# Kernel optimization log

Hardware: AMD Instinct MI355X
Metric: run time of the kernel (lower is better)

## Reference

```python
import jax, jax.numpy as jnp
import numpy as np

N, NFEAT, NHID, OUT, E, P = 50000, 256, 128, 64, 800000, 3
WALK_STEPS, LAMBDA_RW = 13, 0.2


def spmm(row, col, val, x):
    # sparse (N,N) @ dense (N,d) via gather + segment-sum over destination rows
    return jax.ops.segment_sum(val[:, None] * x[col], row, num_segments=N)


def telu(x):
    return x * jnp.tanh(jnp.exp(x))


def setup_inputs() -> dict:
    key = jax.random.key(0)
    ks = jax.random.split(key, 24)
    s = 0.05
    inp = {
        'feature': jax.random.normal(ks[0], (N, NFEAT), jnp.float32),
        'edge_index': jax.random.randint(ks[1], (P, 2, E), 0, N, jnp.int64),
        'edge_val': jax.random.uniform(ks[2], (P, E), jnp.float32) / 16.0,
        'spec_w1': jax.random.normal(ks[3], (P, NFEAT, NHID)) * s,
        'spec_b1': jax.random.normal(ks[4], (P, NHID)) * s,
        'spec_w2': jax.random.normal(ks[5], (P, NHID, OUT)) * s,
        'spec_b2': jax.random.normal(ks[6], (P, OUT)) * s,
        'shared_w1': jax.random.normal(ks[7], (NFEAT, NHID)) * s,
        'shared_b1': jax.random.normal(ks[8], (NHID,)) * s,
        'shared_w2': jax.random.normal(ks[9], (NHID, OUT)) * s,
        'shared_b2': jax.random.normal(ks[10], (OUT,)) * s,
        'weight_b': jax.random.normal(ks[11], (P, 1)) * s,
        'tau': jnp.float32(0.5),
        'mlp_w1': jax.random.normal(ks[12], (OUT * P, NHID)) * s,
        'mlp_b1': jax.random.normal(ks[13], (NHID,)) * s,
        'mlp_w2': jax.random.normal(ks[14], (NHID, OUT)) * s,
        'mlp_b2': jax.random.normal(ks[15], (OUT,)) * s,
        'raw_w1': jax.random.normal(ks[16], (NFEAT, OUT)) * s,
        'raw_b1': jax.random.normal(ks[17], (OUT,)) * s,
        'raw_w2': jax.random.normal(ks[18], (OUT, OUT)) * s,
        'raw_b2': jax.random.normal(ks[19], (OUT,)) * s,
        'proj_w': jax.random.normal(ks[20], (OUT * 4, OUT)) * s,
        'proj_b': jax.random.normal(ks[21], (OUT,)) * s,
    }
    return inp


def reference(feature, edge_index, edge_val, spec_w1, spec_b1, spec_w2, spec_b2,
              shared_w1, shared_b1, shared_w2, shared_b2, weight_b, tau,
              mlp_w1, mlp_b1, mlp_w2, mlp_b2, raw_w1, raw_b1, raw_w2, raw_b2,
              proj_w, proj_b):
    rows = [edge_index[i, 0] for i in range(P)]
    cols = [edge_index[i, 1] for i in range(P)]
    vals = [edge_val[i] for i in range(P)]

    def gc(x, w, b, i):
        return spmm(rows[i], cols[i], vals[i], x @ w) + b

    # path-specific two-layer GCNs (dropout in eval mode = identity)
    specific = []
    for i in range(P):
        h1 = telu(gc(feature, spec_w1[i], spec_b1[i], i))
        specific.append(gc(h1, spec_w2[i], spec_b2[i], i))
    spec_stack = jnp.stack(specific, axis=0)  # (P, N, OUT)

    # shared GCN applied per path
    shared = []
    for i in range(P):
        h1 = telu(gc(feature, shared_w1, shared_b1, i))
        shared.append(gc(h1, shared_w2, shared_b2, i))
    shared_stack = jnp.stack(shared, axis=0)
    H_sh = jnp.mean(shared_stack, axis=0)

    # markov-enhanced path attention
    summaries = []
    for s in specific:
        mean_pool = s.mean(axis=0)
        max_pool = s.max(axis=0)
        p = jax.nn.softmax(s, axis=0)
        entropy = -jnp.sum(p * jnp.log(p + 1e-6), axis=0)
        summaries.append(jnp.concatenate([mean_pool, max_pool, entropy], axis=-1))
    ps = jnp.stack(summaries, axis=0)  # (P, 3*OUT)
    sim = (ps @ ps.T) / (jnp.sqrt(jnp.float32(3 * OUT)) * tau)
    T = jax.nn.softmax(sim, axis=1)
    pi0 = jax.nn.softmax(weight_b.squeeze(-1), axis=0)
    pi = pi0
    for _ in range(WALK_STEPS):
        pi = LAMBDA_RW * pi0 + (1.0 - LAMBDA_RW) * (pi @ T)
    W_tilde = pi[:, None]  # beta dropout is identity in eval mode

    # collaborative MLP on concatenated specific features
    concat_sp = jnp.concatenate(specific, axis=1)  # (N, P*OUT)
    H_col = jax.nn.relu(concat_sp @ mlp_w1 + mlp_b1) @ mlp_w2 + mlp_b2

    # attention-fused specific features
    wprob = jax.nn.softmax(W_tilde, axis=0)[:, 0]  # (P,)
    H_sp_fused = jnp.einsum('pnd,p->nd', spec_stack, wprob)

    # raw path on merged adjacency: final_A = sum_i W_tilde[i] * A_i (applied lazily)
    w = W_tilde[:, 0]

    def merged_spmm(x):
        acc = jnp.zeros((N, x.shape[1]), x.dtype)
        for i in range(P):
            acc = acc + w[i] * spmm(rows[i], cols[i], vals[i], x)
        return acc

    U1 = merged_spmm(feature @ raw_w1) + raw_b1
    U2 = merged_spmm(U1 @ raw_w2) + raw_b2
    H_raw = (U1 + U2) / 2.0

    all_feat = jnp.concatenate([H_sp_fused, H_sh, H_col, H_raw], axis=1)
    out = all_feat @ proj_w + proj_b
    return (out, spec_stack, shared_stack, H_col, H_raw)
```

## Files before the change

### kernel.cpp

```cpp
#include <hip/hip_runtime.h>
#include <hip/hip_bf16.h>
#include <math.h>

#define NN 50000
#define NFEAT 256
#define NHID 128
#define OUTD 64
#define NE 800000
#define NP 3
#define NCH 64
#define RC 782
#define NSB 196
#define NNR (NN + 1)

typedef __hip_bfloat16 bf16;
typedef __attribute__((ext_vector_type(8))) short short8;
typedef __attribute__((ext_vector_type(4))) short short4v;
typedef __attribute__((ext_vector_type(4))) float f32x4;

static inline int cdiv(long a, long b) { return (int)((a + b - 1) / b); }

__device__ __forceinline__ short f2bf(float x) {
    unsigned u = __builtin_bit_cast(unsigned, x);
    unsigned r = (u + 0x7FFFu + ((u >> 16) & 1u)) >> 16;
    return (short)r;
}
__device__ __forceinline__ float bf2f(short b) {
    unsigned u = ((unsigned)(unsigned short)b) << 16;
    return __builtin_bit_cast(float, u);
}

__device__ __forceinline__ void ld8(const float* __restrict__ p, float v[8]) {
    float4 a = *reinterpret_cast<const float4*>(p);
    float4 b = *reinterpret_cast<const float4*>(p + 4);
    v[0] = a.x; v[1] = a.y; v[2] = a.z; v[3] = a.w;
    v[4] = b.x; v[5] = b.y; v[6] = b.z; v[7] = b.w;
}

__device__ __forceinline__ void store4(float* p, const float o[4]) {
    *reinterpret_cast<float4*>(p) = make_float4(o[0], o[1], o[2], o[3]);
}
__device__ __forceinline__ void store4(bf16* p, const float o[4]) {
    short4v u;
    u[0] = f2bf(o[0]); u[1] = f2bf(o[1]); u[2] = f2bf(o[2]); u[3] = f2bf(o[3]);
    *reinterpret_cast<short4v*>(p) = u;
}

__global__ void transpose_split(const float* __restrict__ src, bf16* __restrict__ dh,
                                bf16* __restrict__ dl, int K, int M, long total) {
    long idx = (long)blockIdx.x * blockDim.x + threadIdx.x;
    if (idx >= total) return;
    long pm = idx / K;
    int k = (int)(idx - pm * K);
    long p = pm / M;
    int m = (int)(pm - p * M);
    float v = src[(p * K + k) * M + m];
    short hb = f2bf(v);
    short lb = f2bf(v - bf2f(hb));
    reinterpret_cast<short*>(dh)[idx] = hb;
    reinterpret_cast<short*>(dl)[idx] = lb;
}

template <int K, int M, int MODE, int ACT, typename OT>
__global__ __launch_bounds__(256) void gemm_mfma(
    const float* __restrict__ A, const bf16* __restrict__ Bh, const bf16* __restrict__ Bl,
    const float* __restrict__ bias, OT* __restrict__ out, int nrows,
    const float* __restrict__ wvec, const float* __restrict__ s1,
    const float* __restrict__ s2, const float* __restrict__ s3) {
    constexpr int MC = M / 16;
    __shared__ short AsH[64 * 32];
    __shared__ short AsL[64 * 32];

    int t = threadIdx.x;
    int n0 = blockIdx.x * 64;
    int w = t >> 6;
    int l = t & 63;
    int lr = l & 15, lq = l >> 4;

    float w0 = 0.f, w1 = 0.f, w2 = 0.f;
    if (MODE == 2) { w0 = wvec[3]; w1 = wvec[4]; w2 = wvec[5]; }

    f32x4 acc[MC];
#pragma unroll
    for (int i = 0; i < MC; ++i) {
        f32x4 z = {0.f, 0.f, 0.f, 0.f};
        acc[i] = z;
    }

    int sr = t >> 2, sc = t & 3;
    int gn_s = n0 + sr;
    int wslot = (sc ^ ((sr >> 2) & 3)) << 3;
    short* wpH = &AsH[sr * 32 + wslot];
    short* wpL = &AsL[sr * 32 + wslot];

    int rrow = (w << 4) + lr;
    int roff = rrow * 32 + ((lq ^ ((rrow >> 2) & 3)) << 3);
    const short* rpH = &AsH[roff];
    const short* rpL = &AsL[roff];

    const short* Bhs = reinterpret_cast<const short*>(Bh);
    const short* Bls = reinterpret_cast<const short*>(Bl);

    auto loadA = [&](int k0, float v[8]) {
        if (gn_s >= nrows) {
#pragma unroll
            for (int j = 0; j < 8; ++j) v[j] = 0.f;
            return;
        }
        if (MODE == 0) {
            ld8(A + (long)gn_s * K + k0 + sc * 8, v);
        } else if (MODE == 1) {
            int plane = k0 >> 6;
            int d = (k0 & 63) + sc * 8;
            ld8(A + ((long)plane * NN + gn_s) * OUTD + d, v);
        } else {
            int seg = k0 >> 6;
            int d = (k0 & 63) + sc * 8;
            if (seg == 0) {
                float x0[8], x1[8], x2[8];
                ld8(A + ((long)0 * NN + gn_s) * OUTD + d, x0);
                ld8(A + ((long)1 * NN + gn_s) * OUTD + d, x1);
                ld8(A + ((long)2 * NN + gn_s) * OUTD + d, x2);
#pragma unroll
                for (int j = 0; j < 8; ++j) v[j] = w0 * x0[j] + w1 * x1[j] + w2 * x2[j];
            } else if (seg == 1) {
                float x0[8], x1[8], x2[8];
                ld8(s1 + ((long)0 * NN + gn_s) * OUTD + d, x0);
                ld8(s1 + ((long)1 * NN + gn_s) * OUTD + d, x1);
                ld8(s1 + ((long)2 * NN + gn_s) * OUTD + d, x2);
#pragma unroll
                for (int j = 0; j < 8; ++j) v[j] = (x0[j] + x1[j] + x2[j]) * (1.0f / 3.0f);
            } else if (seg == 2) {
                ld8(s2 + (long)gn_s * OUTD + d, v);
            } else {
                ld8(s3 + (long)gn_s * OUTD + d, v);
            }
        }
    };

    float v[8];
    loadA(0, v);
    for (int k0 = 0; k0 < K; k0 += 32) {
        short8 ah, al;
#pragma unroll
        for (int j = 0; j < 8; ++j) {
            short hb = f2bf(v[j]);
            ah[j] = hb;
            al[j] = f2bf(v[j] - bf2f(hb));
        }
        __syncthreads();
        *reinterpret_cast<short8*>(wpH) = ah;
        *reinterpret_cast<short8*>(wpL) = al;
        __syncthreads();
        if (k0 + 32 < K) loadA(k0 + 32, v);
        short8 fah = *reinterpret_cast<const short8*>(rpH);
        short8 fal = *reinterpret_cast<const short8*>(rpL);
#pragma unroll
        for (int m = 0; m < MC; ++m) {
            long wb = (long)(m * 16 + lr) * K + k0 + (lq << 3);
            short8 bh = *reinterpret_cast<const short8*>(Bhs + wb);
            short8 bl = *reinterpret_cast<const short8*>(Bls + wb);
            acc[m] = __builtin_amdgcn_mfma_f32_16x16x32_bf16(bh, fah, acc[m], 0, 0, 0);
            acc[m] = __builtin_amdgcn_mfma_f32_16x16x32_bf16(bl, fah, acc[m], 0, 0, 0);
            acc[m] = __builtin_amdgcn_mfma_f32_16x16x32_bf16(bh, fal, acc[m], 0, 0, 0);
        }
    }

    int gn = n0 + (w << 4) + lr;
    if (gn < nrows) {
#pragma unroll
        for (int m = 0; m < MC; ++m) {
            int mb = m * 16 + (lq << 2);
            float o[4];
#pragma unroll
            for (int r = 0; r < 4; ++r) {
                o[r] = acc[m][r] + (bias ? bias[mb + r] : 0.f);
                if (ACT == 2) o[r] = fmaxf(o[r], 0.f);
            }
            store4(&out[(long)gn * M + mb], o);
        }
    }
}

__global__ void hist_all(const int* __restrict__ ei, int* __restrict__ cnt) {
    int p = blockIdx.y;
    int e = blockIdx.x * blockDim.x + threadIdx.x;
    if (e >= NE) return;
    int r = ei[((long)p * 2) * NE + e];
    atomicAdd(&cnt[(long)p * NN + r], 1);
}

__global__ void scan_pass1(const int* __restrict__ cnt, int* __restrict__ bsum) {
    int p = blockIdx.y, b = blockIdx.x, t = threadIdx.x;
    int idx = b * 256 + t;
    int v = (idx < NN) ? cnt[(long)p * NN + idx] : 0;
    __shared__ int sh[256];
    sh[t] = v;
    __syncthreads();
    for (int off = 128; off > 0; off >>= 1) {
        if (t < off) sh[t] += sh[t + off];
        __syncthreads();
    }
    if (t == 0) bsum[p * NSB + b] = sh[0];
}

__global__ void scan_pass2(const int* __restrict__ bsum, int* __restrict__ boff) {
    int p = blockIdx.x, t = threadIdx.x;
    int v = (t < NSB) ? bsum[p * NSB + t] : 0;
    __shared__ int sh[256];
    sh[t] = v;
    __syncthreads();
    for (int off = 1; off < 256; off <<= 1) {
        int tmp = (t >= off) ? sh[t - off] : 0;
        __syncthreads();
        sh[t] += tmp;
        __syncthreads();
    }
    if (t < NSB) boff[p * NSB + t] = sh[t] - v;
}

__global__ void scan_pass3(const int* __restrict__ cnt, const int* __restrict__ boff,
                           int* __restrict__ rowptr, int* __restrict__ cursor) {
    int p = blockIdx.y, b = blockIdx.x, t = threadIdx.x;
    int idx = b * 256 + t;
    int v = (idx < NN) ? cnt[(long)p * NN + idx] : 0;
    __shared__ int sh[256];
    sh[t] = v;
    __syncthreads();
    for (int off = 1; off < 256; off <<= 1) {
        int tmp = (t >= off) ? sh[t - off] : 0;
        __syncthreads();
        sh[t] += tmp;
        __syncthreads();
    }
    int rp = boff[p * NSB + b] + sh[t] - v;
    if (idx < NN) {
        rowptr[(long)p * NNR + idx] = rp;
        cursor[(long)p * NN + idx] = rp;
    }
    if (idx == NN - 1) rowptr[(long)p * NNR + NN] = rp + v;
}

__global__ void scatter_all(const int* __restrict__ ei, const float* __restrict__ ev,
                            int* __restrict__ cursor, int* __restrict__ csr_col,
                            float* __restrict__ csr_val) {
    int p = blockIdx.y;
    int e = blockIdx.x * blockDim.x + threadIdx.x;
    if (e >= NE) return;
    int r = ei[((long)p * 2) * NE + e];
    int c = ei[((long)p * 2 + 1) * NE + e];
    float v = ev[(long)p * NE + e];
    int pos = atomicAdd(&cursor[(long)p * NN + r], 1);
    csr_col[(long)p * NE + pos] = c;
    csr_val[(long)p * NE + pos] = v;
}

template <int M, int ACT, int RPB>
__global__ void spmm_dual(const int* __restrict__ rowptr, const int* __restrict__ ccol,
                          const float* __restrict__ cval,
                          const bf16* __restrict__ Ya, const bf16* __restrict__ Yb,
                          const float* __restrict__ biasA, const float* __restrict__ biasB,
                          float* __restrict__ outA, float* __restrict__ outB) {
    constexpr int TPR = M / 2;
    int t = threadIdx.x;
    int n = blockIdx.x * RPB + t / TPR;
    int hs = t % TPR;
    int h = hs * 2;
    if (n >= NN) return;
    int e0 = rowptr[n], e1 = rowptr[n + 1];
    float aAl = biasA[h], aAh = biasA[h + 1];
    float aBl = biasB[h], aBh = biasB[h + 1];
    const unsigned* Ua = reinterpret_cast<const unsigned*>(Ya);
    const unsigned* Ub = reinterpret_cast<const unsigned*>(Yb);
    int e = e0;
    for (; e + 3 < e1; e += 4) {
        int c0 = ccol[e], c1 = ccol[e + 1], c2 = ccol[e + 2], c3 = ccol[e + 3];
        float v0 = cval[e], v1 = cval[e + 1], v2 = cval[e + 2], v3 = cval[e + 3];
        unsigned a0 = Ua[(long)c0 * TPR + hs], a1 = Ua[(long)c1 * TPR + hs];
        unsigned a2 = Ua[(long)c2 * TPR + hs], a3 = Ua[(long)c3 * TPR + hs];
        unsigned b0 = Ub[(long)c0 * TPR + hs], b1 = Ub[(long)c1 * TPR + hs];
        unsigned b2 = Ub[(long)c2 * TPR + hs], b3 = Ub[(long)c3 * TPR + hs];
        aAl += v0 * bf2f((short)a0) + v1 * bf2f((short)a1) + v2 * bf2f((short)a2) + v3 * bf2f((short)a3);
        aAh += v0 * bf2f((short)(a0 >> 16)) + v1 * bf2f((short)(a1 >> 16)) +
               v2 * bf2f((short)(a2 >> 16)) + v3 * bf2f((short)(a3 >> 16));
        aBl += v0 * bf2f((short)b0) + v1 * bf2f((short)b1) + v2 * bf2f((short)b2) + v3 * bf2f((short)b3);
        aBh += v0 * bf2f((short)(b0 >> 16)) + v1 * bf2f((short)(b1 >> 16)) +
               v2 * bf2f((short)(b2 >> 16)) + v3 * bf2f((short)(b3 >> 16));
    }
    for (; e < e1; ++e) {
        int c = ccol[e];
        float v = cval[e];
        unsigned a = Ua[(long)c * TPR + hs];
        unsigned b = Ub[(long)c * TPR + hs];
        aAl += v * bf2f((short)a);
        aAh += v * bf2f((short)(a >> 16));
        aBl += v * bf2f((short)b);
        aBh += v * bf2f((short)(b >> 16));
    }
    if (ACT == 1) {
        aAl = aAl * tanhf(expf(aAl)); aAh = aAh * tanhf(expf(aAh));
        aBl = aBl * tanhf(expf(aBl)); aBh = aBh * tanhf(expf(aBh));
    }
    *reinterpret_cast<float2*>(&outA[(long)n * M + h]) = make_float2(aAl, aAh);
    *reinterpret_cast<float2*>(&outB[(long)n * M + h]) = make_float2(aBl, aBh);
}

__global__ void spmm_merged(const int* __restrict__ rp0, const int* __restrict__ cc0, const float* __restrict__ cv0,
                            const int* __restrict__ rp1, const int* __restrict__ cc1, const float* __restrict__ cv1,
                            const int* __restrict__ rp2, const int* __restrict__ cc2, const float* __restrict__ cv2,
                            const bf16* __restrict__ Y, const float* __restrict__ wvec,
                            const float* __restrict__ bias, float* __restrict__ out) {
    constexpr int TPR = 32;
    int t = threadIdx.x;
    int n = blockIdx.x * 2 + t / TPR;
    int hs = t % TPR;
    int h = hs * 2;
    if (n >= NN) return;
    const int* rps[3] = {rp0, rp1, rp2};
    const int* ccs[3] = {cc0, cc1, cc2};
    const float* cvs[3] = {cv0, cv1, cv2};
    const unsigned* U = reinterpret_cast<const unsigned*>(Y);
    float al = 0.f, ah = 0.f;
#pragma unroll
    for (int p = 0; p < 3; ++p) {
        const int* cc = ccs[p];
        const float* cv = cvs[p];
        int e0 = rps[p][n], e1 = rps[p][n + 1];
        float sl = 0.f, sh = 0.f;
        int e = e0;
        for (; e + 3 < e1; e += 4) {
            int c0 = cc[e], c1 = cc[e + 1], c2 = cc[e + 2], c3 = cc[e + 3];
            float v0 = cv[e], v1 = cv[e + 1], v2 = cv[e + 2], v3 = cv[e + 3];
            unsigned y0 = U[(long)c0 * TPR + hs], y1 = U[(long)c1 * TPR + hs];
            unsigned y2 = U[(long)c2 * TPR + hs], y3 = U[(long)c3 * TPR + hs];
            sl += v0 * bf2f((short)y0) + v1 * bf2f((short)y1) + v2 * bf2f((short)y2) + v3 * bf2f((short)y3);
            sh += v0 * bf2f((short)(y0 >> 16)) + v1 * bf2f((short)(y1 >> 16)) +
                  v2 * bf2f((short)(y2 >> 16)) + v3 * bf2f((short)(y3 >> 16));
        }
        for (; e < e1; ++e) {
            unsigned y = U[(long)cc[e] * TPR + hs];
            float v = cv[e];
            sl += v * bf2f((short)y);
            sh += v * bf2f((short)(y >> 16));
        }
        float wv = wvec[p];
        al += wv * sl;
        ah += wv * sh;
    }
    *reinterpret_cast<float2*>(&out[(long)n * OUTD + h]) =
        make_float2(al + bias[h], ah + bias[h + 1]);
}

__global__ void colsum_passA(const float* __restrict__ spec, float* __restrict__ pmax,
                             float* __restrict__ psum, float* __restrict__ pexp) {
    int p = blockIdx.y, c = blockIdx.x;
    int t = threadIdx.x;
    int d = t & 63, rg = t >> 6;
    const float* base = spec + (long)p * NN * OUTD;
    int r0 = c * RC, r1 = min(r0 + RC, NN);
    float m = -INFINITY, s = 0.f, e = 0.f;
    for (int r = r0 + rg; r < r1; r += 4) {
        float v = base[(long)r * OUTD + d];
        s += v;
        if (v > m) { e = e * __expf(m - v) + 1.0f; m = v; }
        else e += __expf(v - m);
    }
    __shared__ float rm[256], rs[256], re[256];
    rm[t] = m; rs[t] = s; re[t] = e;
    __syncthreads();
    for (int off = 128; off >= 64; off >>= 1) {
        if (t < off) {
            float m2 = fmaxf(rm[t], rm[t + off]);
            re[t] = re[t] * __expf(rm[t] - m2) + re[t + off] * __expf(rm[t + off] - m2);
            rm[t] = m2;
            rs[t] = rs[t] + rs[t + off];
        }
        __syncthreads();
    }
    if (t < 64) {
        long idx = ((long)p * 64 + t) * NCH + c;
        pmax[idx] = rm[t]; psum[idx] = rs[t]; pexp[idx] = re[t];
    }
}

__global__ void colsum_reduceB(const float* __restrict__ pmax, const float* __restrict__ psum,
                               const float* __restrict__ pexp, float* __restrict__ ps,
                               float* __restrict__ zbuf) {
    int b = blockIdx.x;
    int p = b >> 6, d = b & 63;
    int t = threadIdx.x;
    long idx = (long)b * NCH + t;
    float m = pmax[idx], s = psum[idx], e = pexp[idx];
    for (int off = 32; off > 0; off >>= 1) {
        float m2 = fmaxf(m, __shfl_xor(m, off));
        e = e * __expf(m - m2) + __shfl_xor(e, off) * __expf(__shfl_xor(m, off) - m2);
        m = m2;
        s += __shfl_xor(s, off);
    }
    if (t == 0) {
        ps[p * 192 + d] = s / (float)NN;
        ps[p * 192 + 64 + d] = m;
        zbuf[b] = e;
    }
}

__global__ void colsum_passC(const float* __restrict__ spec, const float* __restrict__ ps,
                             const float* __restrict__ zbuf, float* __restrict__ pent) {
    int p = blockIdx.y, c = blockIdx.x;
    int t = threadIdx.x;
    int d = t & 63, rg = t >> 6;
    const float* base = spec + (long)p * NN * OUTD;
    float gm = ps[p * 192 + 64 + d];
    float zinv = 1.0f / zbuf[p * 64 + d];
    int r0 = c * RC, r1 = min(r0 + RC, NN);
    float ent = 0.f;
    for (int r = r0 + rg; r < r1; r += 4) {
        float v = base[(long)r * OUTD + d];
        float pv = __expf(v - gm) * zinv;
        ent -= pv * __logf(pv + 1e-6f);
    }
    __shared__ float rd[256];
    rd[t] = ent;
    __syncthreads();
    for (int off = 128; off >= 64; off >>= 1) {
        if (t < off) rd[t] += rd[t + off];
        __syncthreads();
    }
    if (t < 64) pent[((long)p * 64 + t) * NCH + c] = rd[t];
}

__global__ void colsum_reduceD(const float* __restrict__ pent, float* __restrict__ ps) {
    int b = blockIdx.x;
    int p = b >> 6, d = b & 63;
    int t = threadIdx.x;
    float e = pent[(long)b * NCH + t];
    for (int off = 32; off > 0; off >>= 1) e += __shfl_xor(e, off);
    if (t == 0) ps[p * 192 + 128 + d] = e;
}

__global__ void walk_kernel(const float* __restrict__ ps, const float* __restrict__ weight_b,
                            const float* __restrict__ tau_p, float* __restrict__ wout) {
    if (threadIdx.x != 0 || blockIdx.x != 0) return;
    float sim[3][3];
    float inv = 1.0f / (sqrtf(192.0f) * tau_p[0]);
    for (int i = 0; i < 3; ++i)
        for (int j = 0; j < 3; ++j) {
            float dotv = 0.f;
            for (int k = 0; k < 192; ++k) dotv += ps[i * 192 + k] * ps[j * 192 + k];
            sim[i][j] = dotv * inv;
        }
    float T[3][3];
    for (int i = 0; i < 3; ++i) {
        float m = fmaxf(sim[i][0], fmaxf(sim[i][1], sim[i][2]));
        float e0 = expf(sim[i][0] - m), e1 = expf(sim[i][1] - m), e2 = expf(sim[i][2] - m);
        float s = e0 + e1 + e2;
        T[i][0] = e0 / s; T[i][1] = e1 / s; T[i][2] = e2 / s;
    }
    float b0 = weight_b[0], b1 = weight_b[1], b2 = weight_b[2];
    float m = fmaxf(b0, fmaxf(b1, b2));
    float e0 = expf(b0 - m), e1 = expf(b1 - m), e2 = expf(b2 - m);
    float s = e0 + e1 + e2;
    float pi0[3] = {e0 / s, e1 / s, e2 / s};
    float pi[3] = {pi0[0], pi0[1], pi0[2]};
    for (int it = 0; it < 13; ++it) {
        float n0 = pi[0] * T[0][0] + pi[1] * T[1][0] + pi[2] * T[2][0];
        float n1 = pi[0] * T[0][1] + pi[1] * T[1][1] + pi[2] * T[2][1];
        float n2 = pi[0] * T[0][2] + pi[1] * T[1][2] + pi[2] * T[2][2];
        pi[0] = 0.2f * pi0[0] + 0.8f * n0;
        pi[1] = 0.2f * pi0[1] + 0.8f * n1;
        pi[2] = 0.2f * pi0[2] + 0.8f * n2;
    }
    wout[0] = pi[0]; wout[1] = pi[1]; wout[2] = pi[2];
    float mm = fmaxf(pi[0], fmaxf(pi[1], pi[2]));
    float f0 = expf(pi[0] - mm), f1 = expf(pi[1] - mm), f2 = expf(pi[2] - mm);
    float fs = f0 + f1 + f2;
    wout[3] = f0 / fs; wout[4] = f1 / fs; wout[5] = f2 / fs;
}

__global__ void hraw_final(const float* __restrict__ U1, float* __restrict__ Hraw) {
    long i = (long)blockIdx.x * blockDim.x + threadIdx.x;
    if (i >= (long)NN * OUTD) return;
    Hraw[i] = 0.5f * (U1[i] + Hraw[i]);
}

extern "C" void kernel_launch(void* const* d_in, const int* in_sizes, int n_in,
                              void* d_out, int out_size, void* d_ws, size_t ws_size,
                              hipStream_t stream) {
    const float* feature   = (const float*)d_in[0];
    const int*   edge_index= (const int*)d_in[1];
    const float* edge_val  = (const float*)d_in[2];
    const float* spec_w1   = (const float*)d_in[3];
    const float* spec_b1   = (const float*)d_in[4];
    const float* spec_w2   = (const float*)d_in[5];
    const float* spec_b2   = (const float*)d_in[6];
    const float* shared_w1 = (const float*)d_in[7];
    const float* shared_b1 = (const float*)d_in[8];
    const float* shared_w2 = (const float*)d_in[9];
    const float* shared_b2 = (const float*)d_in[10];
    const float* weight_b  = (const float*)d_in[11];
    const float* tau       = (const float*)d_in[12];
    const float* mlp_w1    = (const float*)d_in[13];
    const float* mlp_b1    = (const float*)d_in[14];
    const float* mlp_w2    = (const float*)d_in[15];
    const float* mlp_b2    = (const float*)d_in[16];
    const float* raw_w1    = (const float*)d_in[17];
    const float* raw_b1    = (const float*)d_in[18];
    const float* raw_w2    = (const float*)d_in[19];
    const float* raw_b2    = (const float*)d_in[20];
    const float* proj_w    = (const float*)d_in[21];
    const float* proj_b    = (const float*)d_in[22];

    float* out        = (float*)d_out;
    float* spec_stack = out + (long)NN * OUTD;
    float* shr_stack  = spec_stack + 3L * NN * OUTD;
    float* Hcol       = out + 7L * NN * OUTD;
    float* Hraw       = out + 8L * NN * OUTD;

    char* wp = (char*)d_ws;
    bf16* XWsh = (bf16*)wp; wp += (long)NN * 128 * sizeof(bf16);
    bf16* XWsp = (bf16*)wp; wp += (long)NN * 128 * sizeof(bf16);
    float* h1sp = (float*)wp; wp += (long)NN * 128 * sizeof(float);
    float* h1sh = (float*)wp; wp += (long)NN * 128 * sizeof(float);
    bf16* Bsp  = (bf16*)wp; wp += (long)NN * OUTD * sizeof(bf16);
    bf16* Bsh  = (bf16*)wp; wp += (long)NN * OUTD * sizeof(bf16);
    float* psBuf = (float*)wp; wp += 1024 * sizeof(float);
    float* wBuf  = (float*)wp; wp += 64 * sizeof(float);
    float* zBuf  = (float*)wp; wp += 256 * sizeof(float);
    float* pMax  = (float*)wp; wp += (long)3 * 64 * NCH * sizeof(float);
    float* pSum  = (float*)wp; wp += (long)3 * 64 * NCH * sizeof(float);
    float* pExp  = (float*)wp; wp += (long)3 * 64 * NCH * sizeof(float);
    float* pEnt  = (float*)wp; wp += (long)3 * 64 * NCH * sizeof(float);
    int*   csr_col_all = (int*)wp;   wp += (long)NP * NE * sizeof(int);
    float* csr_val_all = (float*)wp; wp += (long)NP * NE * sizeof(float);
    int*   rowptr_all  = (int*)wp;   wp += (long)NP * NNR * sizeof(int) + 64;
    int* cnt    = (int*)wp; wp += (long)NP * NN * sizeof(int);
    int* cursor = (int*)wp; wp += (long)NP * NN * sizeof(int);
    int* bsum   = (int*)wp; wp += (long)NP * NSB * sizeof(int);
    int* boff   = (int*)wp; wp += (long)NP * NSB * sizeof(int);
    bf16* w1sp_h = (bf16*)wp; wp += 3L * 256 * 128 * sizeof(bf16);
    bf16* w1sp_l = (bf16*)wp; wp += 3L * 256 * 128 * sizeof(bf16);
    bf16* w1sh_h = (bf16*)wp; wp += 256L * 128 * sizeof(bf16);
    bf16* w1sh_l = (bf16*)wp; wp += 256L * 128 * sizeof(bf16);
    bf16* w2sp_h = (bf16*)wp; wp += 3L * 128 * 64 * sizeof(bf16);
    bf16* w2sp_l = (bf16*)wp; wp += 3L * 128 * 64 * sizeof(bf16);
    bf16* w2sh_h = (bf16*)wp; wp += 128L * 64 * sizeof(bf16);
    bf16* w2sh_l = (bf16*)wp; wp += 128L * 64 * sizeof(bf16);
    bf16* mlp1_h = (bf16*)wp; wp += 192L * 128 * sizeof(bf16);
    bf16* mlp1_l = (bf16*)wp; wp += 192L * 128 * sizeof(bf16);
    bf16* mlp2_h = (bf16*)wp; wp += 128L * 64 * sizeof(bf16);
    bf16* mlp2_l = (bf16*)wp; wp += 128L * 64 * sizeof(bf16);
    bf16* raw1_h = (bf16*)wp; wp += 256L * 64 * sizeof(bf16);
    bf16* raw1_l = (bf16*)wp; wp += 256L * 64 * sizeof(bf16);
    bf16* raw2_h = (bf16*)wp; wp += 64L * 64 * sizeof(bf16);
    bf16* raw2_l = (bf16*)wp; wp += 64L * 64 * sizeof(bf16);
    bf16* proj_h = (bf16*)wp; wp += 256L * 64 * sizeof(bf16);
    bf16* proj_l = (bf16*)wp; wp += 256L * 64 * sizeof(bf16);

    int* rowptr[NP]; int* csr_col[NP]; float* csr_val[NP];
    for (int p = 0; p < NP; ++p) {
        rowptr[p]  = rowptr_all + (long)p * NNR;
        csr_col[p] = csr_col_all + (long)p * NE;
        csr_val[p] = csr_val_all + (long)p * NE;
    }

    const int TB = 256;
    int g_rows = cdiv(NN, 64);

    transpose_split<<<cdiv(3L * 256 * 128, TB), TB, 0, stream>>>(spec_w1, w1sp_h, w1sp_l, 256, 128, 3L * 256 * 128);
    transpose_split<<<cdiv(256L * 128, TB), TB, 0, stream>>>(shared_w1, w1sh_h, w1sh_l, 256, 128, 256L * 128);
    transpose_split<<<cdiv(3L * 128 * 64, TB), TB, 0, stream>>>(spec_w2, w2sp_h, w2sp_l, 128, 64, 3L * 128 * 64);
    transpose_split<<<cdiv(128L * 64, TB), TB, 0, stream>>>(shared_w2, w2sh_h, w2sh_l, 128, 64, 128L * 64);
    transpose_split<<<cdiv(192L * 128, TB), TB, 0, stream>>>(mlp_w1, mlp1_h, mlp1_l, 192, 128, 192L * 128);
    transpose_split<<<cdiv(128L * 64, TB), TB, 0, stream>>>(mlp_w2, mlp2_h, mlp2_l, 128, 64, 128L * 64);
    transpose_split<<<cdiv(256L * 64, TB), TB, 0, stream>>>(raw_w1, raw1_h, raw1_l, 256, 64, 256L * 64);
    transpose_split<<<cdiv(64L * 64, TB), TB, 0, stream>>>(raw_w2, raw2_h, raw2_l, 64, 64, 64L * 64);
    transpose_split<<<cdiv(256L * 64, TB), TB, 0, stream>>>(proj_w, proj_h, proj_l, 256, 64, 256L * 64);

    hipMemsetAsync(cnt, 0, (long)NP * NN * sizeof(int), stream);
    {
        dim3 gE(cdiv(NE, TB), NP);
        hist_all<<<gE, TB, 0, stream>>>(edge_index, cnt);
        dim3 gS(NSB, NP);
        scan_pass1<<<gS, 256, 0, stream>>>(cnt, bsum);
        scan_pass2<<<NP, 256, 0, stream>>>(bsum, boff);
        scan_pass3<<<gS, 256, 0, stream>>>(cnt, boff, rowptr_all, cursor);
        scatter_all<<<gE, TB, 0, stream>>>(edge_index, edge_val, cursor, csr_col_all, csr_val_all);
    }

    gemm_mfma<256, 128, 0, 0, bf16><<<g_rows, 256, 0, stream>>>(
        feature, w1sh_h, w1sh_l, nullptr, XWsh, NN, nullptr, nullptr, nullptr, nullptr);

    for (int p = 0; p < NP; ++p) {
        gemm_mfma<256, 128, 0, 0, bf16><<<g_rows, 256, 0, stream>>>(
            feature, w1sp_h + (long)p * 256 * 128, w1sp_l + (long)p * 256 * 128,
            nullptr, XWsp, NN, nullptr, nullptr, nullptr, nullptr);
        spmm_dual<128, 1, 1><<<NN, 64, 0, stream>>>(rowptr[p], csr_col[p], csr_val[p],
                                                    XWsp, XWsh,
                                                    spec_b1 + (long)p * 128, shared_b1,
                                                    h1sp, h1sh);
        gemm_mfma<128, 64, 0, 0, bf16><<<g_rows, 256, 0, stream>>>(
            h1sp, w2sp_h + (long)p * 128 * 64, w2sp_l + (long)p * 128 * 64,
            nullptr, Bsp, NN, nullptr, nullptr, nullptr, nullptr);
        gemm_mfma<128, 64, 0, 0, bf16><<<g_rows, 256, 0, stream>>>(
            h1sh, w2sh_h, w2sh_l, nullptr, Bsh, NN, nullptr, nullptr, nullptr, nullptr);
        spmm_dual<64, 0, 2><<<cdiv(NN, 2), 64, 0, stream>>>(rowptr[p], csr_col[p], csr_val[p],
                                                            Bsp, Bsh,
                                                            spec_b2 + (long)p * 64, shared_b2,
                                                            spec_stack + (long)p * NN * OUTD,
                                                            shr_stack + (long)p * NN * OUTD);
    }

    {
        dim3 gA(NCH, 3);
        colsum_passA<<<gA, 256, 0, stream>>>(spec_stack, pMax, pSum, pExp);
        colsum_reduceB<<<192, 64, 0, stream>>>(pMax, pSum, pExp, psBuf, zBuf);
        colsum_passC<<<gA, 256, 0, stream>>>(spec_stack, psBuf, zBuf, pEnt);
        colsum_reduceD<<<192, 64, 0, stream>>>(pEnt, psBuf);
    }
    walk_kernel<<<1, 64, 0, stream>>>(psBuf, weight_b, tau, wBuf);

    gemm_mfma<192, 128, 1, 2, float><<<g_rows, 256, 0, stream>>>(
        spec_stack, mlp1_h, mlp1_l, mlp_b1, h1sp, NN, nullptr, nullptr, nullptr, nullptr);
    gemm_mfma<128, 64, 0, 0, float><<<g_rows, 256, 0, stream>>>(
        h1sp, mlp2_h, mlp2_l, mlp_b2, Hcol, NN, nullptr, nullptr, nullptr, nullptr);

    float* U1 = h1sh;
    gemm_mfma<256, 64, 0, 0, bf16><<<g_rows, 256, 0, stream>>>(
        feature, raw1_h, raw1_l, nullptr, Bsp, NN, nullptr, nullptr, nullptr, nullptr);
    spmm_merged<<<cdiv(NN, 2), 64, 0, stream>>>(rowptr[0], csr_col[0], csr_val[0],
                                                rowptr[1], csr_col[1], csr_val[1],
                                                rowptr[2], csr_col[2], csr_val[2],
                                                Bsp, wBuf, raw_b1, U1);
    gemm_mfma<64, 64, 0, 0, bf16><<<g_rows, 256, 0, stream>>>(
        U1, raw2_h, raw2_l, nullptr, Bsh, NN, nullptr, nullptr, nullptr, nullptr);
    spmm_merged<<<cdiv(NN, 2), 64, 0, stream>>>(rowptr[0], csr_col[0], csr_val[0],
                                                rowptr[1], csr_col[1], csr_val[1],
                                                rowptr[2], csr_col[2], csr_val[2],
                                                Bsh, wBuf, raw_b2, Hraw);
    hraw_final<<<cdiv((long)NN * OUTD, TB), TB, 0, stream>>>(U1, Hraw);

    gemm_mfma<256, 64, 2, 0, float><<<g_rows, 256, 0, stream>>>(
        spec_stack, proj_h, proj_l, proj_b, out, NN, wBuf, shr_stack, Hcol, Hraw);
}
```

Before: 1.575 ms.

## Interleave dual SpMM operands, pack CSR col/val pairs, use faster TeLU

The GEMMs that feed the dual SpMM now write their bf16 outputs interleaved, specific and shared values for the same column side by side, so each gather fetches one 64-bit word per edge instead of two 32-bit words from separate arrays. CSR column indices and values are packed into an int2 array so each edge needs one load. TeLU now uses an exp-based tanh formula instead of tanhf. The interleaved store in the GEMM epilogue becomes scalar 2-byte strided writes, which may cost write efficiency.

```diff
diff --git a/kernel.cpp b/kernel.cpp
--- a/kernel.cpp
+++ b/kernel.cpp
@@ -17,6 +17,7 @@
 typedef __attribute__((ext_vector_type(8))) short short8;
 typedef __attribute__((ext_vector_type(4))) short short4v;
 typedef __attribute__((ext_vector_type(4))) float f32x4;
+typedef unsigned long long u64;
 
 static inline int cdiv(long a, long b) { return (int)((a + b - 1) / b); }
 
@@ -28,6 +29,12 @@
 __device__ __forceinline__ float bf2f(short b) {
     unsigned u = ((unsigned)(unsigned short)b) << 16;
     return __builtin_bit_cast(float, u);
+}
+
+__device__ __forceinline__ float telu_f(float x) {
+    float e = __expf(x);
+    float t = __expf(-2.0f * e);
+    return x * (1.0f - t) / (1.0f + t);
 }
 
 __device__ __forceinline__ void ld8(const float* __restrict__ p, float v[8]) {
@@ -61,12 +68,12 @@
     reinterpret_cast<short*>(dl)[idx] = lb;
 }
 
-template <int K, int M, int MODE, int ACT, typename OT>
+template <int K, int M, int MODE, int ACT, typename OT, int ILV>
 __global__ __launch_bounds__(256) void gemm_mfma(
     const float* __restrict__ A, const bf16* __restrict__ Bh, const bf16* __restrict__ Bl,
     const float* __restrict__ bias, OT* __restrict__ out, int nrows,
     const float* __restrict__ wvec, const float* __restrict__ s1,
-    const float* __restrict__ s2, const float* __restrict__ s3) {
+    const float* __restrict__ s2, const float* __restrict__ s3, int ooff) {
     constexpr int MC = M / 16;
     __shared__ short AsH[64 * 32];
     __shared__ short AsL[64 * 32];
@@ -177,7 +184,14 @@
                 o[r] = acc[m][r] + (bias ? bias[mb + r] : 0.f);
                 if (ACT == 2) o[r] = fmaxf(o[r], 0.f);
             }
-            store4(&out[(long)gn * M + mb], o);
+            if (ILV) {
+                short* op = reinterpret_cast<short*>(out);
+#pragma unroll
+                for (int r = 0; r < 4; ++r)
+                    op[(long)gn * (2 * M) + 2 * (mb + r) + ooff] = f2bf(o[r]);
+            } else {
+                store4(&out[(long)gn * M + mb], o);
+            }
         }
     }
 }
@@ -242,8 +256,7 @@
 }
 
 __global__ void scatter_all(const int* __restrict__ ei, const float* __restrict__ ev,
-                            int* __restrict__ cursor, int* __restrict__ csr_col,
-                            float* __restrict__ csr_val) {
+                            int* __restrict__ cursor, int2* __restrict__ csr) {
     int p = blockIdx.y;
     int e = blockIdx.x * blockDim.x + threadIdx.x;
     if (e >= NE) return;
@@ -251,14 +264,12 @@
     int c = ei[((long)p * 2 + 1) * NE + e];
     float v = ev[(long)p * NE + e];
     int pos = atomicAdd(&cursor[(long)p * NN + r], 1);
-    csr_col[(long)p * NE + pos] = c;
-    csr_val[(long)p * NE + pos] = v;
+    csr[(long)p * NE + pos] = make_int2(c, __float_as_int(v));
 }
 
 template <int M, int ACT, int RPB>
-__global__ void spmm_dual(const int* __restrict__ rowptr, const int* __restrict__ ccol,
-                          const float* __restrict__ cval,
-                          const bf16* __restrict__ Ya, const bf16* __restrict__ Yb,
+__global__ void spmm_dual(const int* __restrict__ rowptr, const int2* __restrict__ csr,
+                          const bf16* __restrict__ Yint,
                           const float* __restrict__ biasA, const float* __restrict__ biasB,
                           float* __restrict__ outA, float* __restrict__ outB) {
     constexpr int TPR = M / 2;
@@ -270,44 +281,44 @@
     int e0 = rowptr[n], e1 = rowptr[n + 1];
     float aAl = biasA[h], aAh = biasA[h + 1];
     float aBl = biasB[h], aBh = biasB[h + 1];
-    const unsigned* Ua = reinterpret_cast<const unsigned*>(Ya);
-    const unsigned* Ub = reinterpret_cast<const unsigned*>(Yb);
+    const u64* U = reinterpret_cast<const u64*>(Yint);
     int e = e0;
     for (; e + 3 < e1; e += 4) {
-        int c0 = ccol[e], c1 = ccol[e + 1], c2 = ccol[e + 2], c3 = ccol[e + 3];
-        float v0 = cval[e], v1 = cval[e + 1], v2 = cval[e + 2], v3 = cval[e + 3];
-        unsigned a0 = Ua[(long)c0 * TPR + hs], a1 = Ua[(long)c1 * TPR + hs];
-        unsigned a2 = Ua[(long)c2 * TPR + hs], a3 = Ua[(long)c3 * TPR + hs];
-        unsigned b0 = Ub[(long)c0 * TPR + hs], b1 = Ub[(long)c1 * TPR + hs];
-        unsigned b2 = Ub[(long)c2 * TPR + hs], b3 = Ub[(long)c3 * TPR + hs];
-        aAl += v0 * bf2f((short)a0) + v1 * bf2f((short)a1) + v2 * bf2f((short)a2) + v3 * bf2f((short)a3);
-        aAh += v0 * bf2f((short)(a0 >> 16)) + v1 * bf2f((short)(a1 >> 16)) +
-               v2 * bf2f((short)(a2 >> 16)) + v3 * bf2f((short)(a3 >> 16));
-        aBl += v0 * bf2f((short)b0) + v1 * bf2f((short)b1) + v2 * bf2f((short)b2) + v3 * bf2f((short)b3);
-        aBh += v0 * bf2f((short)(b0 >> 16)) + v1 * bf2f((short)(b1 >> 16)) +
-               v2 * bf2f((short)(b2 >> 16)) + v3 * bf2f((short)(b3 >> 16));
+        int2 p0 = csr[e], p1 = csr[e + 1], p2 = csr[e + 2], p3 = csr[e + 3];
+        u64 u0 = U[(long)p0.x * TPR + hs];
+        u64 u1 = U[(long)p1.x * TPR + hs];
+        u64 u2 = U[(long)p2.x * TPR + hs];
+        u64 u3 = U[(long)p3.x * TPR + hs];
+        float v0 = __int_as_float(p0.y), v1 = __int_as_float(p1.y);
+        float v2 = __int_as_float(p2.y), v3 = __int_as_float(p3.y);
+        aAl += v0 * bf2f((short)u0) + v1 * bf2f((short)u1) + v2 * bf2f((short)u2) + v3 * bf2f((short)u3);
+        aBl += v0 * bf2f((short)(u0 >> 16)) + v1 * bf2f((short)(u1 >> 16)) +
+               v2 * bf2f((short)(u2 >> 16)) + v3 * bf2f((short)(u3 >> 16));
+        aAh += v0 * bf2f((short)(u0 >> 32)) + v1 * bf2f((short)(u1 >> 32)) +
+               v2 * bf2f((short)(u2 >> 32)) + v3 * bf2f((short)(u3 >> 32));
+        aBh += v0 * bf2f((short)(u0 >> 48)) + v1 * bf2f((short)(u1 >> 48)) +
+               v2 * bf2f((short)(u2 >> 48)) + v3 * bf2f((short)(u3 >> 48));
     }
     for (; e < e1; ++e) {
-        int c = ccol[e];
-        float v = cval[e];
-        unsigned a = Ua[(long)c * TPR + hs];
-        unsigned b = Ub[(long)c * TPR + hs];
-        aAl += v * bf2f((short)a);
-        aAh += v * bf2f((short)(a >> 16));
-        aBl += v * bf2f((short)b);
-        aBh += v * bf2f((short)(b >> 16));
+        int2 pe = csr[e];
+        float v = __int_as_float(pe.y);
+        u64 u = U[(long)pe.x * TPR + hs];
+        aAl += v * bf2f((short)u);
+        aBl += v * bf2f((short)(u >> 16));
+        aAh += v * bf2f((short)(u >> 32));
+        aBh += v * bf2f((short)(u >> 48));
     }
     if (ACT == 1) {
-        aAl = aAl * tanhf(expf(aAl)); aAh = aAh * tanhf(expf(aAh));
-        aBl = aBl * tanhf(expf(aBl)); aBh = aBh * tanhf(expf(aBh));
+        aAl = telu_f(aAl); aAh = telu_f(aAh);
+        aBl = telu_f(aBl); aBh = telu_f(aBh);
     }
     *reinterpret_cast<float2*>(&outA[(long)n * M + h]) = make_float2(aAl, aAh);
     *reinterpret_cast<float2*>(&outB[(long)n * M + h]) = make_float2(aBl, aBh);
 }
 
-__global__ void spmm_merged(const int* __restrict__ rp0, const int* __restrict__ cc0, const float* __restrict__ cv0,
-                            const int* __restrict__ rp1, const int* __restrict__ cc1, const float* __restrict__ cv1,
-                            const int* __restrict__ rp2, const int* __restrict__ cc2, const float* __restrict__ cv2,
+__global__ void spmm_merged(const int* __restrict__ rp0, const int2* __restrict__ cs0,
+                            const int* __restrict__ rp1, const int2* __restrict__ cs1,
+                            const int* __restrict__ rp2, const int2* __restrict__ cs2,
                             const bf16* __restrict__ Y, const float* __restrict__ wvec,
                             const float* __restrict__ bias, float* __restrict__ out) {
     constexpr int TPR = 32;
@@ -317,29 +328,29 @@
     int h = hs * 2;
     if (n >= NN) return;
     const int* rps[3] = {rp0, rp1, rp2};
-    const int* ccs[3] = {cc0, cc1, cc2};
-    const float* cvs[3] = {cv0, cv1, cv2};
+    const int2* css[3] = {cs0, cs1, cs2};
     const unsigned* U = reinterpret_cast<const unsigned*>(Y);
     float al = 0.f, ah = 0.f;
 #pragma unroll
     for (int p = 0; p < 3; ++p) {
-        const int* cc = ccs[p];
-        const float* cv = cvs[p];
+        const int2* cs = css[p];
         int e0 = rps[p][n], e1 = rps[p][n + 1];
         float sl = 0.f, sh = 0.f;
         int e = e0;
         for (; e + 3 < e1; e += 4) {
-            int c0 = cc[e], c1 = cc[e + 1], c2 = cc[e + 2], c3 = cc[e + 3];
-            float v0 = cv[e], v1 = cv[e + 1], v2 = cv[e + 2], v3 = cv[e + 3];
-            unsigned y0 = U[(long)c0 * TPR + hs], y1 = U[(long)c1 * TPR + hs];
-            unsigned y2 = U[(long)c2 * TPR + hs], y3 = U[(long)c3 * TPR + hs];
+            int2 p0 = cs[e], p1 = cs[e + 1], p2 = cs[e + 2], p3 = cs[e + 3];
+            unsigned y0 = U[(long)p0.x * TPR + hs], y1 = U[(long)p1.x * TPR + hs];
+            unsigned y2 = U[(long)p2.x * TPR + hs], y3 = U[(long)p3.x * TPR + hs];
+            float v0 = __int_as_float(p0.y), v1 = __int_as_float(p1.y);
+            float v2 = __int_as_float(p2.y), v3 = __int_as_float(p3.y);
             sl += v0 * bf2f((short)y0) + v1 * bf2f((short)y1) + v2 * bf2f((short)y2) + v3 * bf2f((short)y3);
             sh += v0 * bf2f((short)(y0 >> 16)) + v1 * bf2f((short)(y1 >> 16)) +
                   v2 * bf2f((short)(y2 >> 16)) + v3 * bf2f((short)(y3 >> 16));
         }
         for (; e < e1; ++e) {
-            unsigned y = U[(long)cc[e] * TPR + hs];
-            float v = cv[e];
+            int2 pe = cs[e];
+            unsigned y = U[(long)pe.x * TPR + hs];
+            float v = __int_as_float(pe.y);
             sl += v * bf2f((short)y);
             sh += v * bf2f((short)(y >> 16));
         }
@@ -517,12 +528,10 @@
     float* Hraw       = out + 8L * NN * OUTD;
 
     char* wp = (char*)d_ws;
-    bf16* XWsh = (bf16*)wp; wp += (long)NN * 128 * sizeof(bf16);
-    bf16* XWsp = (bf16*)wp; wp += (long)NN * 128 * sizeof(bf16);
+    bf16* XWint = (bf16*)wp; wp += (long)NN * 256 * sizeof(bf16);
+    bf16* Bint  = (bf16*)wp; wp += (long)NN * 128 * sizeof(bf16);
     float* h1sp = (float*)wp; wp += (long)NN * 128 * sizeof(float);
     float* h1sh = (float*)wp; wp += (long)NN * 128 * sizeof(float);
-    bf16* Bsp  = (bf16*)wp; wp += (long)NN * OUTD * sizeof(bf16);
-    bf16* Bsh  = (bf16*)wp; wp += (long)NN * OUTD * sizeof(bf16);
     float* psBuf = (float*)wp; wp += 1024 * sizeof(float);
     float* wBuf  = (float*)wp; wp += 64 * sizeof(float);
     float* zBuf  = (float*)wp; wp += 256 * sizeof(float);
@@ -530,9 +539,8 @@
     float* pSum  = (float*)wp; wp += (long)3 * 64 * NCH * sizeof(float);
     float* pExp  = (float*)wp; wp += (long)3 * 64 * NCH * sizeof(float);
     float* pEnt  = (float*)wp; wp += (long)3 * 64 * NCH * sizeof(float);
-    int*   csr_col_all = (int*)wp;   wp += (long)NP * NE * sizeof(int);
-    float* csr_val_all = (float*)wp; wp += (long)NP * NE * sizeof(float);
-    int*   rowptr_all  = (int*)wp;   wp += (long)NP * NNR * sizeof(int) + 64;
+    int2* csr_all = (int2*)wp;  wp += (long)NP * NE * sizeof(int2);
+    int*  rowptr_all = (int*)wp; wp += (long)NP * NNR * sizeof(int) + 64;
     int* cnt    = (int*)wp; wp += (long)NP * NN * sizeof(int);
     int* cursor = (int*)wp; wp += (long)NP * NN * sizeof(int);
     int* bsum   = (int*)wp; wp += (long)NP * NSB * sizeof(int);
@@ -556,11 +564,10 @@
     bf16* proj_h = (bf16*)wp; wp += 256L * 64 * sizeof(bf16);
     bf16* proj_l = (bf16*)wp; wp += 256L * 64 * sizeof(bf16);
 
-    int* rowptr[NP]; int* csr_col[NP]; float* csr_val[NP];
+    int* rowptr[NP]; int2* csr[NP];
     for (int p = 0; p < NP; ++p) {
-        rowptr[p]  = rowptr_all + (long)p * NNR;
-        csr_col[p] = csr_col_all + (long)p * NE;
-        csr_val[p] = csr_val_all + (long)p * NE;
+        rowptr[p] = rowptr_all + (long)p * NNR;
+        csr[p]    = csr_all + (long)p * NE;
     }
 
     const int TB = 256;
@@ -584,27 +591,25 @@
         scan_pass1<<<gS, 256, 0, stream>>>(cnt, bsum);
         scan_pass2<<<NP, 256, 0, stream>>>(bsum, boff);
         scan_pass3<<<gS, 256, 0, stream>>>(cnt, boff, rowptr_all, cursor);
-        scatter_all<<<gE, TB, 0, stream>>>(edge_index, edge_val, cursor, csr_col_all, csr_val_all);
-    }
-
-    gemm_mfma<256, 128, 0, 0, bf16><<<g_rows, 256, 0, stream>>>(
-        feature, w1sh_h, w1sh_l, nullptr, XWsh, NN, nullptr, nullptr, nullptr, nullptr);
+        scatter_all<<<gE, TB, 0, stream>>>(edge_index, edge_val, cursor, csr_all);
+    }
+
+    gemm_mfma<256, 128, 0, 0, bf16, 1><<<g_rows, 256, 0, stream>>>(
+        feature, w1sh_h, w1sh_l, nullptr, XWint, NN, nullptr, nullptr, nullptr, nullptr, 1);
 
     for (int p = 0; p < NP; ++p) {
-        gemm_mfma<256, 128, 0, 0, bf16><<<g_rows, 256, 0, stream>>>(
+        gemm_mfma<256, 128, 0, 0, bf16, 1><<<g_rows, 256, 0, stream>>>(
             feature, w1sp_h + (long)p * 256 * 128, w1sp_l + (long)p * 256 * 128,
-            nullptr, XWsp, NN, nullptr, nullptr, nullptr, nullptr);
-        spmm_dual<128, 1, 1><<<NN, 64, 0, stream>>>(rowptr[p], csr_col[p], csr_val[p],
-                                                    XWsp, XWsh,
+            nullptr, XWint, NN, nullptr, nullptr, nullptr, nullptr, 0);
+        spmm_dual<128, 1, 1><<<NN, 64, 0, stream>>>(rowptr[p], csr[p], XWint,
                                                     spec_b1 + (long)p * 128, shared_b1,
                                                     h1sp, h1sh);
-        gemm_mfma<128, 64, 0, 0, bf16><<<g_rows, 256, 0, stream>>>(
+        gemm_mfma<128, 64, 0, 0, bf16, 1><<<g_rows, 256, 0, stream>>>(
             h1sp, w2sp_h + (long)p * 128 * 64, w2sp_l + (long)p * 128 * 64,
-            nullptr, Bsp, NN, nullptr, nullptr, nullptr, nullptr);
-        gemm_mfma<128, 64, 0, 0, bf16><<<g_rows, 256, 0, stream>>>(
-            h1sh, w2sh_h, w2sh_l, nullptr, Bsh, NN, nullptr, nullptr, nullptr, nullptr);
-        spmm_dual<64, 0, 2><<<cdiv(NN, 2), 64, 0, stream>>>(rowptr[p], csr_col[p], csr_val[p],
-                                                            Bsp, Bsh,
+            nullptr, Bint, NN, nullptr, nullptr, nullptr, nullptr, 0);
+        gemm_mfma<128, 64, 0, 0, bf16, 1><<<g_rows, 256, 0, stream>>>(
+            h1sh, w2sh_h, w2sh_l, nullptr, Bint, NN, nullptr, nullptr, nullptr, nullptr, 1);
+        spmm_dual<64, 0, 2><<<cdiv(NN, 2), 64, 0, stream>>>(rowptr[p], csr[p], Bint,
                                                             spec_b2 + (long)p * 64, shared_b2,
                                                             spec_stack + (long)p * NN * OUTD,
                                                             shr_stack + (long)p * NN * OUTD);
@@ -619,26 +624,28 @@
     }
     walk_kernel<<<1, 64, 0, stream>>>(psBuf, weight_b, tau, wBuf);
 
-    gemm_mfma<192, 128, 1, 2, float><<<g_rows, 256, 0, stream>>>(
-        spec_stack, mlp1_h, mlp1_l, mlp_b1, h1sp, NN, nullptr, nullptr, nullptr, nullptr);
-    gemm_mfma<128, 64, 0, 0, float><<<g_rows, 256, 0, stream>>>(
-        h1sp, mlp2_h, mlp2_l, mlp_b2, Hcol, NN, nullptr, nullptr, nullptr, nullptr);
+    gemm_mfma<192, 128, 1, 2, float, 0><<<g_rows, 256, 0, stream>>>(
+        spec_stack, mlp1_h, mlp1_l, mlp_b1, h1sp, NN, nullptr, nullptr, nullptr, nullptr, 0);
+    gemm_mfma<128, 64, 0, 0, float, 0><<<g_rows, 256, 0, stream>>>(
+        h1sp, mlp2_h, mlp2_l, mlp_b2, Hcol, NN, nullptr, nullptr, nullptr, nullptr, 0);
 
     float* U1 = h1sh;
-    gemm_mfma<256, 64, 0, 0, bf16><<<g_rows, 256, 0, stream>>>(
-        feature, raw1_h, raw1_l, nullptr, Bsp, NN, nullptr, nullptr, nullptr, nullptr);
-    spmm_merged<<<cdiv(NN, 2), 64, 0, stream>>>(rowptr[0], csr_col[0], csr_val[0],
-                                                rowptr[1], csr_col[1], csr_val[1],
-                                                rowptr[2], csr_col[2], csr_val[2],
-                                                Bsp, wBuf, raw_b1, U1);
-    gemm_mfma<64, 64, 0, 0, bf16><<<g_rows, 256, 0, stream>>>(
-        U1, raw2_h, raw2_l, nullptr, Bsh, NN, nullptr, nullptr, nullptr, nullptr);
-    spmm_merged<<<cdiv(NN, 2), 64, 0, stream>>>(rowptr[0], csr_col[0], csr_val[0],
-                                                rowptr[1], csr_col[1], csr_val[1],
-                                                rowptr[2], csr_col[2], csr_val[2],
-                                                Bsh, wBuf, raw_b2, Hraw);
+    bf16* RB1 = Bint;
+    bf16* RB2 = Bint + (long)NN * OUTD;
+    gemm_mfma<256, 64, 0, 0, bf16, 0><<<g_rows, 256, 0, stream>>>(
+        feature, raw1_h, raw1_l, nullptr, RB1, NN, nullptr, nullptr, nullptr, nullptr, 0);
+    spmm_merged<<<cdiv(NN, 2), 64, 0, stream>>>(rowptr[0], csr[0],
+                                                rowptr[1], csr[1],
+                                                rowptr[2], csr[2],
+                                                RB1, wBuf, raw_b1, U1);
+    gemm_mfma<64, 64, 0, 0, bf16, 0><<<g_rows, 256, 0, stream>>>(
+        U1, raw2_h, raw2_l, nullptr, RB2, NN, nullptr, nullptr, nullptr, nullptr, 0);
+    spmm_merged<<<cdiv(NN, 2), 64, 0, stream>>>(rowptr[0], csr[0],
+                                                rowptr[1], csr[1],
+                                                rowptr[2], csr[2],
+                                                RB2, wBuf, raw_b2, Hraw);
     hraw_final<<<cdiv((long)NN * OUTD, TB), TB, 0, stream>>>(U1, Hraw);
 
-    gemm_mfma<256, 64, 2, 0, float><<<g_rows, 256, 0, stream>>>(
-        spec_stack, proj_h, proj_l, proj_b, out, NN, wBuf, shr_stack, Hcol, Hraw);
-}
+    gemm_mfma<256, 64, 2, 0, float, 0><<<g_rows, 256, 0, stream>>>(
+        spec_stack, proj_h, proj_l, proj_b, out, NN, wBuf, shr_stack, Hcol, Hraw, 0);
+}
```

New measurement: 1.686 ms. 1.07x slower.
